# Kernel tuning notes

Measured on AMD Instinct MI355X. Metric: run time of the kernel, lower is better.

Reference implementation:

```python
import jax, jax.numpy as jnp
import numpy as np

HIDDEN_DIM = 128
NEIGHBOR_K = 2
N_ROWS = 1_000_000
BATCH = 262_144


def setup_inputs() -> dict:
    key = jax.random.key(0)
    k1, k2, k3, k4 = jax.random.split(key, 4)
    D = HIDDEN_DIM
    cat = D * (2 * NEIGHBOR_K + 1)  # 640
    x_rows = jax.random.normal(k1, (N_ROWS, D), dtype=jnp.float32)
    seed_indices = jax.random.randint(k2, (BATCH,), 0, N_ROWS)
    # torch.nn.Linear params: W [out, in], b [out]
    W1 = jax.random.normal(k3, (D, cat), dtype=jnp.float32) * (1.0 / np.sqrt(cat))
    b1 = jnp.zeros((D,), dtype=jnp.float32)
    W2 = jax.random.normal(k4, (D, D), dtype=jnp.float32) * (1.0 / np.sqrt(D))
    b2 = jnp.zeros((D,), dtype=jnp.float32)
    return {"x_rows": x_rows, "seed_indices": seed_indices,
            "W1": W1, "b1": b1, "W2": W2, "b2": b2}


def reference(x_rows, seed_indices, W1, b1, W2, b2):
    N, D = x_rows.shape
    B = seed_indices.shape[0]
    offsets = jnp.arange(-NEIGHBOR_K, NEIGHBOR_K + 1)  # [2k+1]
    idx = jnp.clip(seed_indices[:, None] + offsets[None, :], 0, N - 1)  # [B, 2k+1]
    # gather neighbor rows and flatten -> same as torch.cat(chunks, dim=-1)
    x_cat = x_rows[idx].reshape(B, (2 * NEIGHBOR_K + 1) * D)  # [B, 5D]
    h = jax.nn.relu(x_cat @ W1.T + b1)  # [B, D]
    return h @ W2.T + b2  # [B, D]
```

## Files before the change

kernel.cpp:

```cpp
#include <hip/hip_runtime.h>
#include <hip/hip_bf16.h>

#define D 128
#define CAT 640
#define BM 32
#define KS1 20
#define KS2 4
#define W1F_ELEMS 81920
#define W2F_ELEMS 16384

typedef __attribute__((ext_vector_type(8))) short bf16x8;
typedef __attribute__((ext_vector_type(4))) short short4v;
typedef __attribute__((ext_vector_type(4))) float f32x4;

static __device__ __forceinline__ unsigned short f32_to_bf16(float f) {
    unsigned u = __float_as_uint(f);
    unsigned r = u + 0x7FFFu + ((u >> 16) & 1u);
    return (unsigned short)(r >> 16);
}

__global__ void prep_frags(const float* __restrict__ W1, const float* __restrict__ W2,
                           unsigned short* __restrict__ W1f, unsigned short* __restrict__ W2f) {
    int f = blockIdx.x * 256 + threadIdx.x;
    if (f < W1F_ELEMS) {
        int e = f & 7, l = (f >> 3) & 63, j16 = (f >> 9) & 7, ks = f >> 12;
        int o = j16 * 16 + (l & 15);
        int k = ks * 32 + ((l >> 4) << 3) + e;
        W1f[f] = f32_to_bf16(W1[o * CAT + k]);
    } else if (f < W1F_ELEMS + W2F_ELEMS) {
        int f2 = f - W1F_ELEMS;
        int e = f2 & 7, l = (f2 >> 3) & 63, j16 = (f2 >> 9) & 7, ks = f2 >> 12;
        int o = j16 * 16 + (l & 15);
        int k = ks * 32 + ((l >> 4) << 3) + e;
        W2f[f2] = f32_to_bf16(W2[o * D + k]);
    }
}

__global__ __launch_bounds__(256) void rowmlp_kernel(
    const float* __restrict__ x_rows, const int* __restrict__ seeds,
    const unsigned short* __restrict__ W1f, const float* __restrict__ b1,
    const unsigned short* __restrict__ W2f, const float* __restrict__ b2,
    float* __restrict__ out, int B, int Nrows)
{
    __shared__ __align__(16) unsigned short Abuf[BM * CAT];
    __shared__ __align__(16) unsigned short Hbuf[BM * D];
    __shared__ int sseed[BM];

    const int tid = threadIdx.x;
    const int blk = blockIdx.x;

    if (tid < BM) sseed[tid] = seeds[blk * BM + tid];
    __syncthreads();

    {
        const int lane32 = tid & 31;
        const int segbase = tid >> 5;
        #pragma unroll
        for (int it = 0; it < BM * 5 / 8; ++it) {
            int seg = it * 8 + segbase;
            int row = seg / 5;
            int j = seg - row * 5;
            int idx = sseed[row] + j - 2;
            idx = idx < 0 ? 0 : (idx >= Nrows ? Nrows - 1 : idx);
            float4 v = *((const float4*)(x_rows + (size_t)idx * D) + lane32);
            short4v p;
            p.x = (short)f32_to_bf16(v.x);
            p.y = (short)f32_to_bf16(v.y);
            p.z = (short)f32_to_bf16(v.z);
            p.w = (short)f32_to_bf16(v.w);
            int kshort = j * D + lane32 * 4;
            int off = row * CAT + (kshort ^ ((row & 7) << 3));
            *(short4v*)(&Abuf[off]) = p;
        }
    }
    __syncthreads();

    const int wave = tid >> 6;
    const int l    = tid & 63;
    const int l15  = l & 15;
    const int lhi  = l >> 4;

    f32x4 acc[2][2] = {};
    #pragma unroll
    for (int ks = 0; ks < KS1; ++ks) {
        bf16x8 a[2], b[2];
        #pragma unroll
        for (int m = 0; m < 2; ++m) {
            int row = m * 16 + l15;
            int kshort = ks * 32 + lhi * 8;
            a[m] = *(const bf16x8*)(&Abuf[row * CAT + (kshort ^ ((row & 7) << 3))]);
        }
        #pragma unroll
        for (int n = 0; n < 2; ++n) {
            int j16 = wave * 2 + n;
            b[n] = ((const bf16x8*)W1f)[(ks * 8 + j16) * 64 + l];
        }
        #pragma unroll
        for (int m = 0; m < 2; ++m)
            #pragma unroll
            for (int n = 0; n < 2; ++n)
                acc[m][n] = __builtin_amdgcn_mfma_f32_16x16x32_bf16(a[m], b[n], acc[m][n], 0, 0, 0);
    }

    #pragma unroll
    for (int n = 0; n < 2; ++n) {
        int col = wave * 32 + n * 16 + l15;
        float bias = b1[col];
        #pragma unroll
        for (int m = 0; m < 2; ++m) {
            #pragma unroll
            for (int r = 0; r < 4; ++r) {
                float v = acc[m][n][r] + bias;
                v = v > 0.f ? v : 0.f;
                int row = m * 16 + lhi * 4 + r;
                Hbuf[row * D + (col ^ ((row & 7) << 3))] = f32_to_bf16(v);
            }
        }
    }
    __syncthreads();

    f32x4 acc2[2][2] = {};
    #pragma unroll
    for (int ks = 0; ks < KS2; ++ks) {
        bf16x8 a[2], b[2];
        #pragma unroll
        for (int m = 0; m < 2; ++m) {
            int row = m * 16 + l15;
            int kshort = ks * 32 + lhi * 8;
            a[m] = *(const bf16x8*)(&Hbuf[row * D + (kshort ^ ((row & 7) << 3))]);
        }
        #pragma unroll
        for (int n = 0; n < 2; ++n) {
            int j16 = wave * 2 + n;
            b[n] = ((const bf16x8*)W2f)[(ks * 8 + j16) * 64 + l];
        }
        #pragma unroll
        for (int m = 0; m < 2; ++m)
            #pragma unroll
            for (int n = 0; n < 2; ++n)
                acc2[m][n] = __builtin_amdgcn_mfma_f32_16x16x32_bf16(a[m], b[n], acc2[m][n], 0, 0, 0);
    }

    #pragma unroll
    for (int n = 0; n < 2; ++n) {
        int col = wave * 32 + n * 16 + l15;
        float bias = b2[col];
        #pragma unroll
        for (int m = 0; m < 2; ++m) {
            #pragma unroll
            for (int r = 0; r < 4; ++r) {
                int row = m * 16 + lhi * 4 + r;
                out[(size_t)(blk * BM + row) * D + col] = acc2[m][n][r] + bias;
            }
        }
    }
}

extern "C" void kernel_launch(void* const* d_in, const int* in_sizes, int n_in,
                              void* d_out, int out_size, void* d_ws, size_t ws_size,
                              hipStream_t stream) {
    const float* x_rows = (const float*)d_in[0];
    const int*   seeds  = (const int*)d_in[1];
    const float* W1     = (const float*)d_in[2];
    const float* b1     = (const float*)d_in[3];
    const float* W2     = (const float*)d_in[4];
    const float* b2     = (const float*)d_in[5];
    float* out = (float*)d_out;

    int Nrows = in_sizes[0] / D;
    int B = in_sizes[1];

    unsigned short* W1f = (unsigned short*)d_ws;
    unsigned short* W2f = W1f + W1F_ELEMS;

    prep_frags<<<(W1F_ELEMS + W2F_ELEMS + 255) / 256, 256, 0, stream>>>(W1, W2, W1f, W2f);
    rowmlp_kernel<<<B / BM, 256, 0, stream>>>(x_rows, seeds, W1f, b1, W2f, b2, out, B, Nrows);
}
```

Baseline: 197.2 us.

## Stream neighbor gathers via global_load_lds with double-buffered per-chunk GEMM1 pipeline

Replaces the register-staged gather-and-convert of all five neighbor rows with direct global-to-LDS loads (fp32), double-buffered per neighbor chunk, so the next chunk's gather overlaps MFMA work on the current one. The bf16 conversion moves to the LDS read path just before each MFMA, and H reuses one of the staging buffers. LDS shrinks from about 48KB to 32KB and the launch bounds request 4 blocks, aiming at higher occupancy. In exchange there is a full vmcnt(0) wait plus a barrier per chunk, and conversion work is repeated for every fragment read.

New measurement: 192.6 us. 1.02x faster.

```diff
diff --git a/kernel.cpp b/kernel.cpp
--- a/kernel.cpp
+++ b/kernel.cpp
@@ -4,19 +4,27 @@
 #define D 128
 #define CAT 640
 #define BM 32
-#define KS1 20
-#define KS2 4
 #define W1F_ELEMS 81920
 #define W2F_ELEMS 16384
 
 typedef __attribute__((ext_vector_type(8))) short bf16x8;
-typedef __attribute__((ext_vector_type(4))) short short4v;
 typedef __attribute__((ext_vector_type(4))) float f32x4;
 
 static __device__ __forceinline__ unsigned short f32_to_bf16(float f) {
     unsigned u = __float_as_uint(f);
     unsigned r = u + 0x7FFFu + ((u >> 16) & 1u);
     return (unsigned short)(r >> 16);
+}
+
+static __device__ __forceinline__ unsigned pack_bf16x2(float a, float b) {
+    __hip_bfloat162 h = __float22bfloat162_rn(make_float2(a, b));
+    return *reinterpret_cast<unsigned*>(&h);
+}
+
+static __device__ __forceinline__ void gload_lds16(const float* g, void* lds) {
+    __builtin_amdgcn_global_load_lds(
+        (const __attribute__((address_space(1))) void*)g,
+        (__attribute__((address_space(3))) void*)lds, 16, 0, 0);
 }
 
 __global__ void prep_frags(const float* __restrict__ W1, const float* __restrict__ W2,
@@ -36,14 +44,13 @@
     }
 }
 
-__global__ __launch_bounds__(256) void rowmlp_kernel(
+__global__ __launch_bounds__(256, 4) void rowmlp_kernel(
     const float* __restrict__ x_rows, const int* __restrict__ seeds,
     const unsigned short* __restrict__ W1f, const float* __restrict__ b1,
     const unsigned short* __restrict__ W2f, const float* __restrict__ b2,
-    float* __restrict__ out, int B, int Nrows)
+    float* __restrict__ out, int Nrows)
 {
-    __shared__ __align__(16) unsigned short Abuf[BM * CAT];
-    __shared__ __align__(16) unsigned short Hbuf[BM * D];
+    __shared__ __align__(16) unsigned char smem[2][16384];
     __shared__ int sseed[BM];
 
     const int tid = threadIdx.x;
@@ -52,68 +59,86 @@
     if (tid < BM) sseed[tid] = seeds[blk * BM + tid];
     __syncthreads();
 
-    {
-        const int lane32 = tid & 31;
-        const int segbase = tid >> 5;
-        #pragma unroll
-        for (int it = 0; it < BM * 5 / 8; ++it) {
-            int seg = it * 8 + segbase;
-            int row = seg / 5;
-            int j = seg - row * 5;
-            int idx = sseed[row] + j - 2;
-            idx = idx < 0 ? 0 : (idx >= Nrows ? Nrows - 1 : idx);
-            float4 v = *((const float4*)(x_rows + (size_t)idx * D) + lane32);
-            short4v p;
-            p.x = (short)f32_to_bf16(v.x);
-            p.y = (short)f32_to_bf16(v.y);
-            p.z = (short)f32_to_bf16(v.z);
-            p.w = (short)f32_to_bf16(v.w);
-            int kshort = j * D + lane32 * 4;
-            int off = row * CAT + (kshort ^ ((row & 7) << 3));
-            *(short4v*)(&Abuf[off]) = p;
-        }
-    }
-    __syncthreads();
-
-    const int wave = tid >> 6;
-    const int l    = tid & 63;
-    const int l15  = l & 15;
-    const int lhi  = l >> 4;
+    const int w   = tid >> 6;
+    const int l   = tid & 63;
+    const int l15 = l & 15;
+    const int lhi = l >> 4;
+
+    int sbase[4], scoff[4];
+    #pragma unroll
+    for (int i = 0; i < 4; ++i) {
+        int r = 8 * w + 2 * i + (l >> 5);
+        sbase[i] = sseed[r];
+        scoff[i] = ((l & 31) ^ (r & 7)) << 2;
+    }
+
+#define ISSUE(J)                                                               \
+    {                                                                          \
+        _Pragma("unroll")                                                      \
+        for (int i = 0; i < 4; ++i) {                                          \
+            int idx = sbase[i] + (J) - 2;                                      \
+            idx = idx < 0 ? 0 : (idx >= Nrows ? Nrows - 1 : idx);              \
+            gload_lds16(x_rows + (size_t)idx * D + scoff[i],                   \
+                        (void*)(smem[(J) & 1] + w * 4096 + i * 1024));         \
+        }                                                                      \
+    }
+
+    ISSUE(0)
+
+    const bf16x8* W1v = (const bf16x8*)W1f;
+    const bf16x8* W2v = (const bf16x8*)W2f;
 
     f32x4 acc[2][2] = {};
-    #pragma unroll
-    for (int ks = 0; ks < KS1; ++ks) {
-        bf16x8 a[2], b[2];
-        #pragma unroll
-        for (int m = 0; m < 2; ++m) {
-            int row = m * 16 + l15;
-            int kshort = ks * 32 + lhi * 8;
-            a[m] = *(const bf16x8*)(&Abuf[row * CAT + (kshort ^ ((row & 7) << 3))]);
-        }
-        #pragma unroll
-        for (int n = 0; n < 2; ++n) {
-            int j16 = wave * 2 + n;
-            b[n] = ((const bf16x8*)W1f)[(ks * 8 + j16) * 64 + l];
-        }
-        #pragma unroll
-        for (int m = 0; m < 2; ++m)
-            #pragma unroll
-            for (int n = 0; n < 2; ++n)
-                acc[m][n] = __builtin_amdgcn_mfma_f32_16x16x32_bf16(a[m], b[n], acc[m][n], 0, 0, 0);
-    }
-
+
+    #pragma unroll
+    for (int j = 0; j < 5; ++j) {
+        asm volatile("s_waitcnt vmcnt(0)" ::: "memory");
+        __builtin_amdgcn_s_barrier();
+        if (j < 4) ISSUE(j + 1)
+
+        const float* buf = (const float*)smem[j & 1];
+        #pragma unroll
+        for (int ks = 0; ks < 4; ++ks) {
+            bf16x8 a[2];
+            #pragma unroll
+            for (int m = 0; m < 2; ++m) {
+                const int r = m * 16 + l15;
+                const int s = r & 7;
+                const int cc = ks * 8 + lhi * 2;
+                float4 q0 = *(const float4*)(buf + r * 128 + (((cc) ^ s) << 2));
+                float4 q1 = *(const float4*)(buf + r * 128 + (((cc + 1) ^ s) << 2));
+                union { unsigned u[4]; bf16x8 v; } pk;
+                pk.u[0] = pack_bf16x2(q0.x, q0.y);
+                pk.u[1] = pack_bf16x2(q0.z, q0.w);
+                pk.u[2] = pack_bf16x2(q1.x, q1.y);
+                pk.u[3] = pack_bf16x2(q1.z, q1.w);
+                a[m] = pk.v;
+            }
+            #pragma unroll
+            for (int n = 0; n < 2; ++n) {
+                const int j16 = w * 2 + n;
+                bf16x8 b = W1v[((j * 4 + ks) * 8 + j16) * 64 + l];
+                #pragma unroll
+                for (int m = 0; m < 2; ++m)
+                    acc[m][n] = __builtin_amdgcn_mfma_f32_16x16x32_bf16(a[m], b, acc[m][n], 0, 0, 0);
+            }
+        }
+    }
+#undef ISSUE
+
+    unsigned short (*Hb)[D] = (unsigned short (*)[D])smem[1];
     #pragma unroll
     for (int n = 0; n < 2; ++n) {
-        int col = wave * 32 + n * 16 + l15;
-        float bias = b1[col];
+        const int col = w * 32 + n * 16 + l15;
+        const float bias = b1[col];
         #pragma unroll
         for (int m = 0; m < 2; ++m) {
             #pragma unroll
             for (int r = 0; r < 4; ++r) {
                 float v = acc[m][n][r] + bias;
                 v = v > 0.f ? v : 0.f;
-                int row = m * 16 + lhi * 4 + r;
-                Hbuf[row * D + (col ^ ((row & 7) << 3))] = f32_to_bf16(v);
+                const int row = m * 16 + lhi * 4 + r;
+                Hb[row][col ^ ((row & 7) << 3)] = f32_to_bf16(v);
             }
         }
     }
@@ -121,35 +146,34 @@
 
     f32x4 acc2[2][2] = {};
     #pragma unroll
-    for (int ks = 0; ks < KS2; ++ks) {
-        bf16x8 a[2], b[2];
+    for (int ks = 0; ks < 4; ++ks) {
+        bf16x8 a2[2], bb[2];
         #pragma unroll
         for (int m = 0; m < 2; ++m) {
-            int row = m * 16 + l15;
-            int kshort = ks * 32 + lhi * 8;
-            a[m] = *(const bf16x8*)(&Hbuf[row * D + (kshort ^ ((row & 7) << 3))]);
+            const int row = m * 16 + l15;
+            a2[m] = *(const bf16x8*)(&Hb[row][(ks * 32 + lhi * 8) ^ ((row & 7) << 3)]);
         }
         #pragma unroll
         for (int n = 0; n < 2; ++n) {
-            int j16 = wave * 2 + n;
-            b[n] = ((const bf16x8*)W2f)[(ks * 8 + j16) * 64 + l];
+            const int j16 = w * 2 + n;
+            bb[n] = W2v[(ks * 8 + j16) * 64 + l];
         }
         #pragma unroll
         for (int m = 0; m < 2; ++m)
             #pragma unroll
             for (int n = 0; n < 2; ++n)
-                acc2[m][n] = __builtin_amdgcn_mfma_f32_16x16x32_bf16(a[m], b[n], acc2[m][n], 0, 0, 0);
+                acc2[m][n] = __builtin_amdgcn_mfma_f32_16x16x32_bf16(a2[m], bb[n], acc2[m][n], 0, 0, 0);
     }
 
     #pragma unroll
     for (int n = 0; n < 2; ++n) {
-        int col = wave * 32 + n * 16 + l15;
-        float bias = b2[col];
+        const int col = w * 32 + n * 16 + l15;
+        const float bias = b2[col];
         #pragma unroll
         for (int m = 0; m < 2; ++m) {
             #pragma unroll
             for (int r = 0; r < 4; ++r) {
-                int row = m * 16 + lhi * 4 + r;
+                const int row = m * 16 + lhi * 4 + r;
                 out[(size_t)(blk * BM + row) * D + col] = acc2[m][n][r] + bias;
             }
         }
@@ -174,5 +198,5 @@
     unsigned short* W2f = W1f + W1F_ELEMS;
 
     prep_frags<<<(W1F_ELEMS + W2F_ELEMS + 255) / 256, 256, 0, stream>>>(W1, W2, W1f, W2f);
-    rowmlp_kernel<<<B / BM, 256, 0, stream>>>(x_rows, seeds, W1f, b1, W2f, b2, out, B, Nrows);
-}
+    rowmlp_kernel<<<B / BM, 256, 0, stream>>>(x_rows, seeds, W1f, b1, W2f, b2, out, Nrows);
+}
```
